# Kernel tuning notes

Measured on AMD Instinct MI355X. Metric: run time of the kernel, lower is better.

Reference implementation:

```python
import jax, jax.numpy as jnp
import numpy as np
import math

B, H, S, D = 4, 8, 2048, 64

def setup_inputs() -> dict:
    key = jax.random.key(0)
    k1, k2, k3, k4 = jax.random.split(key, 4)
    query = jax.random.normal(k1, (B, H, S, D), dtype=jnp.float32)
    key_t = jax.random.normal(k2, (B, H, S, D), dtype=jnp.float32)
    value = jax.random.normal(k3, (B, H, S, D), dtype=jnp.float32)
    mask = jax.random.randint(k4, (B, 1, S, S), 0, 2, dtype=jnp.int32)
    return {"query": query, "key": key_t, "value": value, "mask": mask}

def reference(query, key, value, mask):
    d = query.shape[-1]
    # Non-standard score: exp(QK^T) / sqrt(d), then masked fill, then softmax.
    logits = jnp.einsum('bhqd,bhkd->bhqk', query, key)
    scores = jnp.exp(logits) / math.sqrt(d)
    scores = jnp.where(mask == 0, jnp.float32(-1e9), scores)
    p_attn = jax.nn.softmax(scores, axis=-1)
    out = jnp.einsum('bhqk,bhkd->bhqd', p_attn, value)
    return out, p_attn
```

## Files before the change

### kernel.cpp

```cpp
#include <hip/hip_runtime.h>

#define NB 4
#define NH 8
#define NS 2048
#define ND 64
#define NBH (NB * NH)

typedef float f32x4  __attribute__((ext_vector_type(4)));
typedef float f32x16 __attribute__((ext_vector_type(16)));
typedef short s16x8  __attribute__((ext_vector_type(8)));
typedef unsigned int u32;

constexpr int TQ = 128;
constexpr int TK = 128;
constexpr int NT = NS / TK;
constexpr int NZ = 2;

constexpr size_t PM_BYTES  = (size_t)NB * NS * (NS / 8);
constexpr size_t WSL_BYTES = 1 << 20;
constexpr size_t KHL_OFF   = PM_BYTES + WSL_BYTES;
constexpr size_t KHL_BYTES = (size_t)NBH * NT * 32768;
constexpr size_t QHI_OFF   = KHL_OFF + KHL_BYTES;
constexpr size_t QP_BYTES  = (size_t)NBH * NS * ND * 2;
constexpr size_t QLO_OFF   = QHI_OFF + QP_BYTES;
constexpr size_t REC_OFF   = QLO_OFF + QP_BYTES;
constexpr size_t REC_BYTES = (size_t)NBH * NS * NZ * 16;
constexpr size_t WS_NEED   = REC_OFF + REC_BYTES;

__device__ __forceinline__ u32 bf16_rne(u32 u) {
    return (u + 0x7FFFu + ((u >> 16) & 1u)) >> 16;
}
__device__ __forceinline__ void cvt_split(float x, u32 &hi, u32 &lo) {
    u32 h = bf16_rne(__float_as_uint(x));
    float hf = __uint_as_float(h << 16);
    lo = bf16_rne(__float_as_uint(x - hf));
    hi = h;
}

__global__ __launch_bounds__(256)
void pack_maskT_kernel(const int* __restrict__ mask, u32* __restrict__ pmT)
{
    int idx = blockIdx.x * 256 + threadIdx.x;
    int ks = idx & 3;
    int q  = (idx >> 2) & 2047;
    int kt = (idx >> 13) & 15;
    int b  = idx >> 17;
    const int* mp = mask + ((size_t)b * NS + q) * NS + kt * 128 + ks * 32;
    u32 v = 0;
    #pragma unroll
    for (int i = 0; i < 8; ++i) {
        int4 a = *(const int4*)(mp + i * 4);
        v |= (u32)(a.x != 0) << (i * 4)
           | (u32)(a.y != 0) << (i * 4 + 1)
           | (u32)(a.z != 0) << (i * 4 + 2)
           | (u32)(a.w != 0) << (i * 4 + 3);
    }
    pmT[idx] = v;
}

__global__ __launch_bounds__(256)
void ksplit_kernel(const float* __restrict__ K, short* __restrict__ khl)
{
    int idx = blockIdx.x * 256 + threadIdx.x;
    int oct = idx & 7;
    int kg  = (idx >> 3) & 2047;
    int bh  = idx >> 14;
    const float* src = K + ((size_t)bh * NS + kg) * ND + oct * 8;
    f32x4 a = *(const f32x4*)src;
    f32x4 b = *(const f32x4*)(src + 4);
    u32 h[8], lo[8];
    cvt_split(a.x,h[0],lo[0]); cvt_split(a.y,h[1],lo[1]);
    cvt_split(a.z,h[2],lo[2]); cvt_split(a.w,h[3],lo[3]);
    cvt_split(b.x,h[4],lo[4]); cvt_split(b.y,h[5],lo[5]);
    cvt_split(b.z,h[6],lo[6]); cvt_split(b.w,h[7],lo[7]);
    union { u32 u[4]; s16x8 s; } H, L;
    #pragma unroll
    for (int e = 0; e < 4; ++e) {
        H.u[e] = h[2*e]  | (h[2*e+1]  << 16);
        L.u[e] = lo[2*e] | (lo[2*e+1] << 16);
    }
    int kt = kg >> 7, key = kg & 127, d_ = oct >> 1, hl = oct & 1;
    size_t base = (size_t)(bh * NT + kt) * 16384;
    size_t frag = (size_t)(((d_ * 2 + hl) * 128) + key) * 8;
    *(s16x8*)(khl + base + frag)        = H.s;
    *(s16x8*)(khl + base + 8192 + frag) = L.s;
}

__global__ __launch_bounds__(256)
void qsplit_kernel(const float* __restrict__ Q, short* __restrict__ qhi,
                   short* __restrict__ qlo)
{
    int idx = blockIdx.x * 256 + threadIdx.x;
    int oct = idx & 7;
    size_t row = (size_t)(idx >> 3);
    const float* src = Q + row * ND + oct * 8;
    f32x4 a = *(const f32x4*)src;
    f32x4 b = *(const f32x4*)(src + 4);
    u32 h[8], lo[8];
    cvt_split(a.x,h[0],lo[0]); cvt_split(a.y,h[1],lo[1]);
    cvt_split(a.z,h[2],lo[2]); cvt_split(a.w,h[3],lo[3]);
    cvt_split(b.x,h[4],lo[4]); cvt_split(b.y,h[5],lo[5]);
    cvt_split(b.z,h[6],lo[6]); cvt_split(b.w,h[7],lo[7]);
    union { u32 u[4]; s16x8 s; } H, L;
    #pragma unroll
    for (int e = 0; e < 4; ++e) {
        H.u[e] = h[2*e]  | (h[2*e+1]  << 16);
        L.u[e] = lo[2*e] | (lo[2*e+1] << 16);
    }
    *(s16x8*)(qhi + row * ND + oct * 8) = H.s;
    *(s16x8*)(qlo + row * ND + oct * 8) = L.s;
}

__global__ __launch_bounds__(256, 4)
void qk5_kernel(const short* __restrict__ khl,
                const short* __restrict__ qhi,
                const short* __restrict__ qlo,
                const u32* __restrict__ pmT,
                float* __restrict__ p,
                float4* __restrict__ rec)
{
    const int t  = threadIdx.x;
    const int l  = t & 63;
    const int wv = t >> 6;
    const int hl = l >> 5;
    const int ln = l & 31;
    const int bh = blockIdx.x;
    const int b  = bh >> 3;
    const int q0 = blockIdx.y * TQ;
    const int z  = blockIdx.z;
    const int kt0 = z * (NT / NZ);

    float* slab = p + ((size_t)bh * NS + q0 + z * 64) * NS;
    const int q = q0 + wv * 32 + ln;

    s16x8 qh[4], ql[4];
    {
        const short* qr_h = qhi + ((size_t)bh * NS + q) * ND + hl * 8;
        const short* qr_l = qlo + ((size_t)bh * NS + q) * ND + hl * 8;
        #pragma unroll
        for (int d_ = 0; d_ < 4; ++d_) {
            qh[d_] = *(const s16x8*)(qr_h + d_ * 16);
            ql[d_] = *(const s16x8*)(qr_l + d_ * 16);
        }
    }

    const short* kh_head = khl + (size_t)(bh * NT) * 16384;
    const u32*   mrow    = pmT + (size_t)b * (NT * NS * 4) + (size_t)q * 4;

    uint4 mv = *(const uint4*)(mrow + (size_t)kt0 * (NS * 4));
    float m1 = -1e30f, m2 = -1e30f;
    int   i1 = 0;

    for (int kt = kt0, it = 0; it < NT / NZ; ++kt, ++it) {
        {
            f32x4* base = (f32x4*)(slab + (size_t)it * 16384) + t;
            f32x4 z4 = {0.f, 0.f, 0.f, 0.f};
            #pragma unroll
            for (int i = 0; i < 16; ++i)
                __builtin_nontemporal_store(z4, base + i * 256);
        }

        uint4 mv_n = mv;
        if (it + 1 < NT / NZ)
            mv_n = *(const uint4*)(mrow + (size_t)(kt + 1) * (NS * 4));

        const short* kb = kh_head + (size_t)kt * 16384;
        u32 mwv[4] = { mv.x >> (hl * 4), mv.y >> (hl * 4),
                       mv.z >> (hl * 4), mv.w >> (hl * 4) };

        auto top2 = [&](const f32x16& A, int ks) {
            u32 ws = mwv[ks];
            int kbase = kt * 128 + ks * 32 + hl * 4;
            #pragma unroll
            for (int r = 0; r < 16; ++r) {
                int bp = (r & 3) + 8 * (r >> 2);
                float v = ((ws >> bp) & 1u) ? A[r] : -1e30f;
                bool gt = v > m1;
                m2 = gt ? m1 : fmaxf(m2, v);
                m1 = fmaxf(m1, v);
                i1 = gt ? (kbase + bp) : i1;
            }
        };

        #pragma unroll
        for (int kp = 0; kp < 2; ++kp) {
            f32x16 acc0, acc1;
            #pragma unroll
            for (int r = 0; r < 16; ++r) { acc0[r] = 0.f; acc1[r] = 0.f; }
            #pragma unroll
            for (int d_ = 0; d_ < 4; ++d_) {
                const short* fr = kb + (size_t)((((d_ * 2 + hl) * 128) + kp * 64 + ln) * 8);
                s16x8 ah0 = *(const s16x8*)fr;
                s16x8 al0 = *(const s16x8*)(fr + 8192);
                s16x8 ah1 = *(const s16x8*)(fr + 256);
                s16x8 al1 = *(const s16x8*)(fr + 8192 + 256);
                acc0 = __builtin_amdgcn_mfma_f32_32x32x16_bf16(ah0, qh[d_], acc0, 0,0,0);
                acc1 = __builtin_amdgcn_mfma_f32_32x32x16_bf16(ah1, qh[d_], acc1, 0,0,0);
                acc0 = __builtin_amdgcn_mfma_f32_32x32x16_bf16(al0, qh[d_], acc0, 0,0,0);
                acc1 = __builtin_amdgcn_mfma_f32_32x32x16_bf16(al1, qh[d_], acc1, 0,0,0);
                acc0 = __builtin_amdgcn_mfma_f32_32x32x16_bf16(ah0, ql[d_], acc0, 0,0,0);
                acc1 = __builtin_amdgcn_mfma_f32_32x32x16_bf16(ah1, ql[d_], acc1, 0,0,0);
            }
            top2(acc0, kp * 2);
            top2(acc1, kp * 2 + 1);
        }

        mv = mv_n;
    }

    {
        float om1 = __shfl_xor(m1, 32, 64);
        float om2 = __shfl_xor(m2, 32, 64);
        int   oi1 = __shfl_xor(i1, 32, 64);
        float nm1, nm2; int ni1;
        if (om1 > m1)      { nm1 = om1; ni1 = oi1; nm2 = fmaxf(om2, m1); }
        else if (om1 < m1) { nm1 = m1;  ni1 = i1;  nm2 = fmaxf(m2, om1); }
        else { nm1 = m1; ni1 = i1; nm2 = (oi1 == i1) ? fmaxf(m2, om2) : m1; }
        m1 = nm1; i1 = ni1; m2 = nm2;
    }

    if (l < 32) {
        int row = bh * NS + q0 + wv * 32 + ln;
        rec[(size_t)row * NZ + z] = make_float4(m1, m2, __int_as_float(i1), 0.f);
    }
}

__global__ __launch_bounds__(256)
void finish_kernel(const float4* __restrict__ rec,
                   const float* __restrict__ V,
                   float* __restrict__ outp, float* __restrict__ p,
                   int* __restrict__ wsl, int wscap)
{
    int u = blockIdx.x * 256 + threadIdx.x;
    int row = u >> 4, c4 = u & 15;
    float4 r0 = rec[(size_t)row * NZ];
    float4 r1 = rec[(size_t)row * NZ + 1];
    float m1, m2; int i1;
    int j0 = __float_as_int(r0.z), j1 = __float_as_int(r1.z);
    if (r0.x > r1.x)      { m1 = r0.x; i1 = j0; m2 = fmaxf(r0.y, r1.x); }
    else if (r0.x < r1.x) { m1 = r1.x; i1 = j1; m2 = fmaxf(r1.y, r0.x); }
    else { m1 = r0.x; i1 = j0; m2 = (j1 == i1) ? fmaxf(r0.y, r1.y) : m1; }

    float s1 = __expf(m1) * 0.125f;
    float s2 = __expf(m2) * 0.125f;
    bool clean = (m1 > -1e29f) && (s1 < 1e38f) && (s1 - s2 > 15.0f)
                 && (m1 - m2 > 1e-3f);
    int bh = row >> 11;
    if (clean) {
        const float* vr = V + ((size_t)bh * NS + i1) * ND;
        *(f32x4*)(outp + (size_t)row * ND + c4 * 4) = *(const f32x4*)(vr + c4 * 4);
        if (c4 == 0) p[(size_t)row * NS + i1] = 1.0f;
    } else if (c4 == 0 && wscap > 0) {
        int idx = atomicAdd(wsl, 1);
        if (idx < wscap) wsl[1 + idx] = row;
    }
}

__global__ __launch_bounds__(256)
void slow_rows_kernel(const float* __restrict__ Q, const float* __restrict__ K,
                      const float* __restrict__ V, const int* __restrict__ mask,
                      float* __restrict__ outp, float* __restrict__ p,
                      const int* __restrict__ wsl, int wscap, int allrows)
{
    __shared__ float qr[ND];
    __shared__ float redm[4], redz[4];
    __shared__ float ol[ND];
    int n;
    if (allrows) n = NBH * NS;
    else { n = wsl[0]; if (n > wscap) n = wscap; }
    const int t = threadIdx.x;
    const int lane = t & 63, w = t >> 6;

    for (int ii = blockIdx.x; ii < n; ii += gridDim.x) {
        int row = allrows ? ii : wsl[1 + ii];
        int bh = row >> 11, qq = row & (NS - 1), b = bh >> 3;
        const float* Qr = Q + (size_t)row * ND;
        const float* Kb = K + (size_t)bh * NS * ND;
        const float* Vb = V + (size_t)bh * NS * ND;
        const int*   mr = mask + (size_t)b * NS * NS + (size_t)qq * NS;

        __syncthreads();
        if (t < 16) ((float4*)qr)[t] = ((const float4*)Qr)[t];
        if (t < ND) ol[t] = 0.f;
        __syncthreads();

        float sc[8];
        int k0 = t * 8;
        #pragma unroll
        for (int i = 0; i < 8; ++i) {
            const float* kr = Kb + (size_t)(k0 + i) * ND;
            float a = 0.f;
            for (int d = 0; d < ND; d += 4) {
                float4 kv = *(const float4*)(kr + d);
                a += qr[d] * kv.x; a += qr[d + 1] * kv.y;
                a += qr[d + 2] * kv.z; a += qr[d + 3] * kv.w;
            }
            sc[i] = mr[k0 + i] ? __expf(a) * 0.125f : -1e9f;
        }
        float m = sc[0];
        #pragma unroll
        for (int i = 1; i < 8; ++i) m = fmaxf(m, sc[i]);
        #pragma unroll
        for (int d = 1; d < 64; d <<= 1) m = fmaxf(m, __shfl_xor(m, d, 64));
        if (lane == 0) redm[w] = m;
        __syncthreads();
        m = fmaxf(fmaxf(redm[0], redm[1]), fmaxf(redm[2], redm[3]));

        float e[8]; float z = 0.f;
        #pragma unroll
        for (int i = 0; i < 8; ++i) { e[i] = __expf(sc[i] - m); z += e[i]; }
        #pragma unroll
        for (int d = 1; d < 64; d <<= 1) z += __shfl_xor(z, d, 64);
        if (lane == 0) redz[w] = z;
        __syncthreads();
        float Z = redz[0] + redz[1] + redz[2] + redz[3];
        float inv = 1.f / Z;

        float* pr = p + (size_t)row * NS + k0;
        float4 o0, o1;
        o0.x = e[0] * inv; o0.y = e[1] * inv; o0.z = e[2] * inv; o0.w = e[3] * inv;
        o1.x = e[4] * inv; o1.y = e[5] * inv; o1.z = e[6] * inv; o1.w = e[7] * inv;
        *(float4*)pr = o0; *(float4*)(pr + 4) = o1;

        #pragma unroll
        for (int i = 0; i < 8; ++i) {
            float pv = e[i] * inv;
            if (pv > 0.f) {
                const float* vr = Vb + (size_t)(k0 + i) * ND;
                for (int d = 0; d < ND; ++d) atomicAdd(&ol[d], pv * vr[d]);
            }
        }
        __syncthreads();
        if (t < ND) outp[(size_t)row * ND + t] = ol[t];
    }
}

extern "C" void kernel_launch(void* const* d_in, const int* in_sizes, int n_in,
                              void* d_out, int out_size, void* d_ws, size_t ws_size,
                              hipStream_t stream)
{
    const float* Q    = (const float*)d_in[0];
    const float* K    = (const float*)d_in[1];
    const float* V    = (const float*)d_in[2];
    const int*   mask = (const int*)d_in[3];
    float* outp = (float*)d_out;
    float* p    = outp + (size_t)NBH * NS * ND;

    if (ws_size < WS_NEED) {
        slow_rows_kernel<<<dim3(4096), 256, 0, stream>>>(Q, K, V, mask, outp, p,
                                                         nullptr, 0, 1);
        return;
    }

    u32* pmT   = (u32*)d_ws;
    int* wsl   = (int*)((char*)d_ws + PM_BYTES);
    int wscap  = (int)(WSL_BYTES / 4 - 1);
    short* khl = (short*)((char*)d_ws + KHL_OFF);
    short* qhi = (short*)((char*)d_ws + QHI_OFF);
    short* qlo = (short*)((char*)d_ws + QLO_OFF);
    float4* rec = (float4*)((char*)d_ws + REC_OFF);

    hipMemsetAsync(wsl, 0, 4, stream);
    pack_maskT_kernel<<<dim3(2048), 256, 0, stream>>>(mask, pmT);
    ksplit_kernel<<<dim3(2048), 256, 0, stream>>>(K, khl);
    qsplit_kernel<<<dim3(2048), 256, 0, stream>>>(Q, qhi, qlo);

    dim3 grid(NBH, NS / TQ, NZ);
    qk5_kernel<<<grid, 256, 0, stream>>>(khl, qhi, qlo, pmT, p, rec);

    finish_kernel<<<dim3(NBH * NS * 16 / 256), 256, 0, stream>>>(rec, V, outp, p,
                                                                 wsl, wscap);
    slow_rows_kernel<<<dim3(128), 256, 0, stream>>>(Q, K, V, mask, outp, p,
                                                    wsl, wscap, 0);
}
```

Before: 178.3 us.

## Fuse prep kernels into one launch and split key range four ways

The mask packing, K split and Q split kernels, plus the workspace counter memset, are merged into a single prep kernel that dispatches on block index. This removes several launch gaps. The QK top-2 kernel is templated on the number of key splits and uses 4 instead of 2 when the workspace is large enough. That doubles the grid, so each block handles a shorter key range and a smaller slab of p to zero. The finish kernel merges a variable number of partial records, at the cost of more record traffic and a slightly different tie-handling rule.

Result: faster. 174.4 us (-2.2%).

```diff
diff --git a/kernel.cpp b/kernel.cpp
--- a/kernel.cpp
+++ b/kernel.cpp
@@ -14,7 +14,6 @@
 constexpr int TQ = 128;
 constexpr int TK = 128;
 constexpr int NT = NS / TK;
-constexpr int NZ = 2;
 
 constexpr size_t PM_BYTES  = (size_t)NB * NS * (NS / 8);
 constexpr size_t WSL_BYTES = 1 << 20;
@@ -24,8 +23,10 @@
 constexpr size_t QP_BYTES  = (size_t)NBH * NS * ND * 2;
 constexpr size_t QLO_OFF   = QHI_OFF + QP_BYTES;
 constexpr size_t REC_OFF   = QLO_OFF + QP_BYTES;
-constexpr size_t REC_BYTES = (size_t)NBH * NS * NZ * 16;
-constexpr size_t WS_NEED   = REC_OFF + REC_BYTES;
+constexpr size_t REC4_BYTES= (size_t)NBH * NS * 4 * 16;
+constexpr size_t REC2_BYTES= (size_t)NBH * NS * 2 * 16;
+constexpr size_t WS_NEED4  = REC_OFF + REC4_BYTES;
+constexpr size_t WS_NEED2  = REC_OFF + REC2_BYTES;
 
 __device__ __forceinline__ u32 bf16_rne(u32 u) {
     return (u + 0x7FFFu + ((u >> 16) & 1u)) >> 16;
@@ -38,81 +39,81 @@
 }
 
 __global__ __launch_bounds__(256)
-void pack_maskT_kernel(const int* __restrict__ mask, u32* __restrict__ pmT)
-{
-    int idx = blockIdx.x * 256 + threadIdx.x;
-    int ks = idx & 3;
-    int q  = (idx >> 2) & 2047;
-    int kt = (idx >> 13) & 15;
-    int b  = idx >> 17;
-    const int* mp = mask + ((size_t)b * NS + q) * NS + kt * 128 + ks * 32;
-    u32 v = 0;
-    #pragma unroll
-    for (int i = 0; i < 8; ++i) {
-        int4 a = *(const int4*)(mp + i * 4);
-        v |= (u32)(a.x != 0) << (i * 4)
-           | (u32)(a.y != 0) << (i * 4 + 1)
-           | (u32)(a.z != 0) << (i * 4 + 2)
-           | (u32)(a.w != 0) << (i * 4 + 3);
-    }
-    pmT[idx] = v;
-}
-
-__global__ __launch_bounds__(256)
-void ksplit_kernel(const float* __restrict__ K, short* __restrict__ khl)
-{
-    int idx = blockIdx.x * 256 + threadIdx.x;
-    int oct = idx & 7;
-    int kg  = (idx >> 3) & 2047;
-    int bh  = idx >> 14;
-    const float* src = K + ((size_t)bh * NS + kg) * ND + oct * 8;
-    f32x4 a = *(const f32x4*)src;
-    f32x4 b = *(const f32x4*)(src + 4);
-    u32 h[8], lo[8];
-    cvt_split(a.x,h[0],lo[0]); cvt_split(a.y,h[1],lo[1]);
-    cvt_split(a.z,h[2],lo[2]); cvt_split(a.w,h[3],lo[3]);
-    cvt_split(b.x,h[4],lo[4]); cvt_split(b.y,h[5],lo[5]);
-    cvt_split(b.z,h[6],lo[6]); cvt_split(b.w,h[7],lo[7]);
-    union { u32 u[4]; s16x8 s; } H, L;
-    #pragma unroll
-    for (int e = 0; e < 4; ++e) {
-        H.u[e] = h[2*e]  | (h[2*e+1]  << 16);
-        L.u[e] = lo[2*e] | (lo[2*e+1] << 16);
-    }
-    int kt = kg >> 7, key = kg & 127, d_ = oct >> 1, hl = oct & 1;
-    size_t base = (size_t)(bh * NT + kt) * 16384;
-    size_t frag = (size_t)(((d_ * 2 + hl) * 128) + key) * 8;
-    *(s16x8*)(khl + base + frag)        = H.s;
-    *(s16x8*)(khl + base + 8192 + frag) = L.s;
-}
-
-__global__ __launch_bounds__(256)
-void qsplit_kernel(const float* __restrict__ Q, short* __restrict__ qhi,
-                   short* __restrict__ qlo)
-{
-    int idx = blockIdx.x * 256 + threadIdx.x;
-    int oct = idx & 7;
-    size_t row = (size_t)(idx >> 3);
-    const float* src = Q + row * ND + oct * 8;
-    f32x4 a = *(const f32x4*)src;
-    f32x4 b = *(const f32x4*)(src + 4);
-    u32 h[8], lo[8];
-    cvt_split(a.x,h[0],lo[0]); cvt_split(a.y,h[1],lo[1]);
-    cvt_split(a.z,h[2],lo[2]); cvt_split(a.w,h[3],lo[3]);
-    cvt_split(b.x,h[4],lo[4]); cvt_split(b.y,h[5],lo[5]);
-    cvt_split(b.z,h[6],lo[6]); cvt_split(b.w,h[7],lo[7]);
-    union { u32 u[4]; s16x8 s; } H, L;
-    #pragma unroll
-    for (int e = 0; e < 4; ++e) {
-        H.u[e] = h[2*e]  | (h[2*e+1]  << 16);
-        L.u[e] = lo[2*e] | (lo[2*e+1] << 16);
-    }
-    *(s16x8*)(qhi + row * ND + oct * 8) = H.s;
-    *(s16x8*)(qlo + row * ND + oct * 8) = L.s;
-}
-
+void prep_kernel(const int* __restrict__ mask, u32* __restrict__ pmT,
+                 const float* __restrict__ K, short* __restrict__ khl,
+                 const float* __restrict__ Q, short* __restrict__ qhi,
+                 short* __restrict__ qlo, int* __restrict__ wsl)
+{
+    const int bid = blockIdx.x;
+    if (bid == 0 && threadIdx.x == 0) wsl[0] = 0;
+
+    if (bid < 2048) {
+        int idx = bid * 256 + threadIdx.x;
+        int ks = idx & 3;
+        int q  = (idx >> 2) & 2047;
+        int kt = (idx >> 13) & 15;
+        int b  = idx >> 17;
+        const int* mp = mask + ((size_t)b * NS + q) * NS + kt * 128 + ks * 32;
+        u32 v = 0;
+        #pragma unroll
+        for (int i = 0; i < 8; ++i) {
+            int4 a = *(const int4*)(mp + i * 4);
+            v |= (u32)(a.x != 0) << (i * 4)
+               | (u32)(a.y != 0) << (i * 4 + 1)
+               | (u32)(a.z != 0) << (i * 4 + 2)
+               | (u32)(a.w != 0) << (i * 4 + 3);
+        }
+        pmT[idx] = v;
+    } else if (bid < 4096) {
+        int idx = (bid - 2048) * 256 + threadIdx.x;
+        int oct = idx & 7;
+        int kg  = (idx >> 3) & 2047;
+        int bh  = idx >> 14;
+        const float* src = K + ((size_t)bh * NS + kg) * ND + oct * 8;
+        f32x4 a = *(const f32x4*)src;
+        f32x4 b = *(const f32x4*)(src + 4);
+        u32 h[8], lo[8];
+        cvt_split(a.x,h[0],lo[0]); cvt_split(a.y,h[1],lo[1]);
+        cvt_split(a.z,h[2],lo[2]); cvt_split(a.w,h[3],lo[3]);
+        cvt_split(b.x,h[4],lo[4]); cvt_split(b.y,h[5],lo[5]);
+        cvt_split(b.z,h[6],lo[6]); cvt_split(b.w,h[7],lo[7]);
+        union { u32 u[4]; s16x8 s; } H, L;
+        #pragma unroll
+        for (int e = 0; e < 4; ++e) {
+            H.u[e] = h[2*e]  | (h[2*e+1]  << 16);
+            L.u[e] = lo[2*e] | (lo[2*e+1] << 16);
+        }
+        int kt = kg >> 7, key = kg & 127, d_ = oct >> 1, hl = oct & 1;
+        size_t base = (size_t)(bh * NT + kt) * 16384;
+        size_t frag = (size_t)(((d_ * 2 + hl) * 128) + key) * 8;
+        *(s16x8*)(khl + base + frag)        = H.s;
+        *(s16x8*)(khl + base + 8192 + frag) = L.s;
+    } else {
+        int idx = (bid - 4096) * 256 + threadIdx.x;
+        int oct = idx & 7;
+        size_t row = (size_t)(idx >> 3);
+        const float* src = Q + row * ND + oct * 8;
+        f32x4 a = *(const f32x4*)src;
+        f32x4 b = *(const f32x4*)(src + 4);
+        u32 h[8], lo[8];
+        cvt_split(a.x,h[0],lo[0]); cvt_split(a.y,h[1],lo[1]);
+        cvt_split(a.z,h[2],lo[2]); cvt_split(a.w,h[3],lo[3]);
+        cvt_split(b.x,h[4],lo[4]); cvt_split(b.y,h[5],lo[5]);
+        cvt_split(b.z,h[6],lo[6]); cvt_split(b.w,h[7],lo[7]);
+        union { u32 u[4]; s16x8 s; } H, L;
+        #pragma unroll
+        for (int e = 0; e < 4; ++e) {
+            H.u[e] = h[2*e]  | (h[2*e+1]  << 16);
+            L.u[e] = lo[2*e] | (lo[2*e+1] << 16);
+        }
+        *(s16x8*)(qhi + row * ND + oct * 8) = H.s;
+        *(s16x8*)(qlo + row * ND + oct * 8) = L.s;
+    }
+}
+
+template<int NZT>
 __global__ __launch_bounds__(256, 4)
-void qk5_kernel(const short* __restrict__ khl,
+void qk6_kernel(const short* __restrict__ khl,
                 const short* __restrict__ qhi,
                 const short* __restrict__ qlo,
                 const u32* __restrict__ pmT,
@@ -128,9 +129,12 @@
     const int b  = bh >> 3;
     const int q0 = blockIdx.y * TQ;
     const int z  = blockIdx.z;
-    const int kt0 = z * (NT / NZ);
-
-    float* slab = p + ((size_t)bh * NS + q0 + z * 64) * NS;
+    const int kt0 = z * (NT / NZT);
+    constexpr int NIT = NT / NZT;
+    constexpr int ZROWS = TQ / NZT;
+
+    float* slab = p + ((size_t)bh * NS + q0 + z * ZROWS) * NS;
+    constexpr int SLAB_F4_PER_IT = ZROWS * NS / 4 / NIT;
     const int q = q0 + wv * 32 + ln;
 
     s16x8 qh[4], ql[4];
@@ -151,17 +155,17 @@
     float m1 = -1e30f, m2 = -1e30f;
     int   i1 = 0;
 
-    for (int kt = kt0, it = 0; it < NT / NZ; ++kt, ++it) {
+    for (int kt = kt0, it = 0; it < NIT; ++kt, ++it) {
         {
-            f32x4* base = (f32x4*)(slab + (size_t)it * 16384) + t;
+            f32x4* base = (f32x4*)slab + (size_t)it * SLAB_F4_PER_IT + t;
             f32x4 z4 = {0.f, 0.f, 0.f, 0.f};
             #pragma unroll
-            for (int i = 0; i < 16; ++i)
+            for (int i = 0; i < SLAB_F4_PER_IT / 256; ++i)
                 __builtin_nontemporal_store(z4, base + i * 256);
         }
 
         uint4 mv_n = mv;
-        if (it + 1 < NT / NZ)
+        if (it + 1 < NIT)
             mv_n = *(const uint4*)(mrow + (size_t)(kt + 1) * (NS * 4));
 
         const short* kb = kh_head + (size_t)kt * 16384;
@@ -221,10 +225,11 @@
 
     if (l < 32) {
         int row = bh * NS + q0 + wv * 32 + ln;
-        rec[(size_t)row * NZ + z] = make_float4(m1, m2, __int_as_float(i1), 0.f);
-    }
-}
-
+        rec[(size_t)row * NZT + z] = make_float4(m1, m2, __int_as_float(i1), 0.f);
+    }
+}
+
+template<int NZT>
 __global__ __launch_bounds__(256)
 void finish_kernel(const float4* __restrict__ rec,
                    const float* __restrict__ V,
@@ -233,13 +238,18 @@
 {
     int u = blockIdx.x * 256 + threadIdx.x;
     int row = u >> 4, c4 = u & 15;
-    float4 r0 = rec[(size_t)row * NZ];
-    float4 r1 = rec[(size_t)row * NZ + 1];
-    float m1, m2; int i1;
-    int j0 = __float_as_int(r0.z), j1 = __float_as_int(r1.z);
-    if (r0.x > r1.x)      { m1 = r0.x; i1 = j0; m2 = fmaxf(r0.y, r1.x); }
-    else if (r0.x < r1.x) { m1 = r1.x; i1 = j1; m2 = fmaxf(r1.y, r0.x); }
-    else { m1 = r0.x; i1 = j0; m2 = (j1 == i1) ? fmaxf(r0.y, r1.y) : m1; }
+    float4 r0 = rec[(size_t)row * NZT];
+    float m1 = r0.x, m2 = r0.y;
+    int   i1 = __float_as_int(r0.z);
+    #pragma unroll
+    for (int zz = 1; zz < NZT; ++zz) {
+        float4 rz = rec[(size_t)row * NZT + zz];
+        float a = rz.x;
+        int   j = __float_as_int(rz.z);
+        if (a > m1)      { m2 = fmaxf(rz.y, m1); m1 = a; i1 = j; }
+        else if (a < m1) { m2 = fmaxf(m2, a); }
+        else             { m2 = m1; }
+    }
 
     float s1 = __expf(m1) * 0.125f;
     float s2 = __expf(m2) * 0.125f;
@@ -346,7 +356,7 @@
     float* outp = (float*)d_out;
     float* p    = outp + (size_t)NBH * NS * ND;
 
-    if (ws_size < WS_NEED) {
+    if (ws_size < WS_NEED2) {
         slow_rows_kernel<<<dim3(4096), 256, 0, stream>>>(Q, K, V, mask, outp, p,
                                                          nullptr, 0, 1);
         return;
@@ -360,16 +370,19 @@
     short* qlo = (short*)((char*)d_ws + QLO_OFF);
     float4* rec = (float4*)((char*)d_ws + REC_OFF);
 
-    hipMemsetAsync(wsl, 0, 4, stream);
-    pack_maskT_kernel<<<dim3(2048), 256, 0, stream>>>(mask, pmT);
-    ksplit_kernel<<<dim3(2048), 256, 0, stream>>>(K, khl);
-    qsplit_kernel<<<dim3(2048), 256, 0, stream>>>(Q, qhi, qlo);
-
-    dim3 grid(NBH, NS / TQ, NZ);
-    qk5_kernel<<<grid, 256, 0, stream>>>(khl, qhi, qlo, pmT, p, rec);
-
-    finish_kernel<<<dim3(NBH * NS * 16 / 256), 256, 0, stream>>>(rec, V, outp, p,
-                                                                 wsl, wscap);
+    prep_kernel<<<dim3(6144), 256, 0, stream>>>(mask, pmT, K, khl, Q, qhi, qlo, wsl);
+
+    if (ws_size >= WS_NEED4) {
+        dim3 grid(NBH, NS / TQ, 4);
+        qk6_kernel<4><<<grid, 256, 0, stream>>>(khl, qhi, qlo, pmT, p, rec);
+        finish_kernel<4><<<dim3(NBH * NS * 16 / 256), 256, 0, stream>>>(
+            rec, V, outp, p, wsl, wscap);
+    } else {
+        dim3 grid(NBH, NS / TQ, 2);
+        qk6_kernel<2><<<grid, 256, 0, stream>>>(khl, qhi, qlo, pmT, p, rec);
+        finish_kernel<2><<<dim3(NBH * NS * 16 / 256), 256, 0, stream>>>(
+            rec, V, outp, p, wsl, wscap);
+    }
     slow_rows_kernel<<<dim3(128), 256, 0, stream>>>(Q, K, V, mask, outp, p,
                                                     wsl, wscap, 0);
 }
```
